# Kernel tuning notes

Hardware: AMD Instinct MI355X
Metric: run time of the kernel (lower is better)

## Reference

```python
import jax, jax.numpy as jnp
import numpy as np

N = 50000   # nodes
E = 800000  # edges (avg degree 16)
H = 128     # hidden_channels
G = 50      # num_gaussians
CUT = 6.0   # cutoff
PI = float(np.pi)
SHIFT = float(np.log(2.0))


def ssp(x):
    # ShiftedSoftplus
    return jax.nn.softplus(x) - SHIFT


def setup_inputs() -> dict:
    key = jax.random.key(0)
    ks = jax.random.split(key, 32)
    p = lambda k, shape: jax.random.normal(k, shape, jnp.float32) * 0.05
    inp = {
        "z": jax.random.normal(ks[0], (N, 3), jnp.float32),
        "dist": jax.random.uniform(ks[1], (E,), jnp.float32) * CUT,
        "edge_index": jax.random.randint(ks[2], (2, E), 0, N, dtype=jnp.int32),
        "init_w": p(ks[3], (3, H)), "init_b": jnp.zeros((H,), jnp.float32),
        # layer 0
        "e0_lin_w": p(ks[4], (H, H)),
        "e0_m0_w": p(ks[5], (G, H)), "e0_m0_b": jnp.zeros((H,), jnp.float32),
        "e0_m2_w": p(ks[6], (H, H)), "e0_m2_b": jnp.zeros((H,), jnp.float32),
        "v0_l1_w": p(ks[7], (H, H)), "v0_l1_b": jnp.zeros((H,), jnp.float32),
        "v0_l2_w": p(ks[8], (H, H)), "v0_l2_b": jnp.zeros((H,), jnp.float32),
        # layer 1
        "e1_lin_w": p(ks[9], (H, H)),
        "e1_m0_w": p(ks[10], (G, H)), "e1_m0_b": jnp.zeros((H,), jnp.float32),
        "e1_m2_w": p(ks[11], (H, H)), "e1_m2_b": jnp.zeros((H,), jnp.float32),
        "v1_l1_w": p(ks[12], (H, H)), "v1_l1_b": jnp.zeros((H,), jnp.float32),
        "v1_l2_w": p(ks[13], (H, H)), "v1_l2_b": jnp.zeros((H,), jnp.float32),
        # readout
        "u_l1_w": p(ks[14], (H, H)), "u_l1_b": jnp.zeros((H,), jnp.float32),
        "u_l2_w": p(ks[15], (H, 3)), "u_l2_b": jnp.zeros((3,), jnp.float32),
    }
    return inp


def reference(z, dist, edge_index, init_w, init_b,
              e0_lin_w, e0_m0_w, e0_m0_b, e0_m2_w, e0_m2_b,
              v0_l1_w, v0_l1_b, v0_l2_w, v0_l2_b,
              e1_lin_w, e1_m0_w, e1_m0_b, e1_m2_w, e1_m2_b,
              v1_l1_w, v1_l1_b, v1_l2_w, v1_l2_b,
              u_l1_w, u_l1_b, u_l2_w, u_l2_b):
    n = z.shape[0]
    j, i = edge_index[0], edge_index[1]  # source, target

    # RBF embedding of dist.to(long)  (torch truncates toward zero)
    offset = jnp.linspace(0.0, CUT, G, dtype=jnp.float32)
    coeff = -0.5 / (offset[1] - offset[0]) ** 2
    demb = jnp.exp(coeff * (jnp.trunc(dist)[:, None] - offset[None, :]) ** 2)  # [E,G]

    # cosine cutoff gate
    C = 0.5 * (jnp.cos(dist * (PI / CUT)) + 1.0)  # [E]

    v = z @ init_w + init_b  # [N,H]

    layers = [
        (e0_lin_w, e0_m0_w, e0_m0_b, e0_m2_w, e0_m2_b, v0_l1_w, v0_l1_b, v0_l2_w, v0_l2_b),
        (e1_lin_w, e1_m0_w, e1_m0_b, e1_m2_w, e1_m2_b, v1_l1_w, v1_l1_b, v1_l2_w, v1_l2_b),
    ]
    for lin_w, m0_w, m0_b, m2_w, m2_b, l1_w, l1_b, l2_w, l2_b in layers:
        # update_e: filter MLP on RBF, gated by cutoff, times gathered node feats
        W = (ssp(demb @ m0_w + m0_b) @ m2_w + m2_b) * C[:, None]  # [E,H]
        e = (v @ lin_w)[j] * W                                     # [E,H]
        # update_v: scatter-add into target nodes, then node MLP + residual
        agg = jax.ops.segment_sum(e, i, num_segments=n)            # [N,H]
        v = v + (ssp(agg @ l1_w + l1_b) @ l2_w + l2_b)

    # update_u readout
    return ssp(v @ u_l1_w + u_l1_b) @ u_l2_w + u_l2_b  # [N,3]
```

## Files before the change

### kernel.cpp

```cpp
#include <hip/hip_runtime.h>
#include <cstdint>
#include <cstddef>

#define HD 128
#define GD 50
static constexpr float PI_F   = 3.14159265358979323846f;
static constexpr float CUTF   = 6.0f;
static constexpr float SHIFTF = 0.69314718055994530942f;

typedef _Float16 f16x8 __attribute__((ext_vector_type(8)));
typedef _Float16 f16x2 __attribute__((ext_vector_type(2)));
typedef float    f32x4 __attribute__((ext_vector_type(4)));

struct Ptr8 { const float* p[8]; };

__device__ __forceinline__ float ssp(float x) {
    float e = __expf(-fabsf(x));
    return fmaxf(x, 0.0f) + __logf(1.0f + e) - SHIFTF;
}

__device__ __forceinline__ _Float16* t16(_Float16* base, int row, int byte) {
    return (_Float16*)((char*)base + row * 256 + (byte ^ ((row & 7) << 4)));
}

__device__ __forceinline__ void mfma32(const f16x8 af[4],
                                       const _Float16* __restrict__ Bf,
                                       int lane, f32x4 acc[8]) {
    #pragma unroll
    for (int ks = 0; ks < 4; ++ks)
        #pragma unroll
        for (int ct = 0; ct < 8; ++ct)
            acc[ct] = __builtin_amdgcn_mfma_f32_16x16x32_f16(
                af[ks], ((const f16x8*)Bf)[(ct * 4 + ks) * 64 + lane], acc[ct], 0, 0, 0);
}

template <int ACT>
__device__ __forceinline__ void acc_to_t16(const f32x4 acc[8], const float* bias,
                                           int lane, _Float16* tile) {
    int col0 = lane & 15, r0 = (lane >> 4) * 4;
    #pragma unroll
    for (int ct = 0; ct < 8; ++ct) {
        int c = ct * 16 + col0;
        float bs = bias ? bias[c] : 0.f;
        #pragma unroll
        for (int r = 0; r < 4; ++r) {
            float o = acc[ct][r] + bs;
            if (ACT) o = ssp(o);
            *t16(tile, r0 + r, c * 2) = (_Float16)o;
        }
    }
}

__device__ __forceinline__ void t16_to_af(_Float16* tile, int lane, f16x8 af[4]) {
    int row = lane & 15, kgB = (lane >> 4) * 16;
    #pragma unroll
    for (int ks = 0; ks < 4; ++ks)
        af[ks] = *(const f16x8*)t16(tile, row, ks * 64 + kgB);
}

__device__ __forceinline__ void t16_store(_Float16* tile, _Float16* g,
                                          int rowbase, int lane, int n) {
    #pragma unroll
    for (int it = 0; it < 4; ++it) {
        int f8 = it * 64 + lane;
        int row = f8 >> 4, g8 = f8 & 15;
        f16x8 h = *(const f16x8*)t16(tile, row, g8 * 16);
        if (rowbase + row < n) ((f16x8*)g)[(size_t)(rowbase + row) * 16 + g8] = h;
    }
}

__device__ __forceinline__ void vz_acc(const float* __restrict__ z,
                                       const float* __restrict__ iw,
                                       const float* __restrict__ ib,
                                       int rowbase, int lane, int n,
                                       f32x4 vz[8]) {
    int col0 = lane & 15, r0 = (lane >> 4) * 4;
    float zr[4][3];
    #pragma unroll
    for (int r = 0; r < 4; ++r) {
        int row = min(rowbase + r0 + r, n - 1);
        zr[r][0] = z[row * 3 + 0];
        zr[r][1] = z[row * 3 + 1];
        zr[r][2] = z[row * 3 + 2];
    }
    #pragma unroll
    for (int ct = 0; ct < 8; ++ct) {
        int c = ct * 16 + col0;
        float w0 = iw[c], w1 = iw[HD + c], w2 = iw[2 * HD + c], bz = ib[c];
        #pragma unroll
        for (int r = 0; r < 4; ++r)
            vz[ct][r] = fmaf(zr[r][0], w0, fmaf(zr[r][1], w1, fmaf(zr[r][2], w2, bz)));
    }
}

__global__ __launch_bounds__(HD) void k_wtab2(Ptr8 P, float* __restrict__ wtab) {
    const int bin = blockIdx.x, layer = blockIdx.y;
    const int t = threadIdx.x;
    const float* m0w = P.p[layer * 4 + 0];
    const float* m0b = P.p[layer * 4 + 1];
    const float* m2w = P.p[layer * 4 + 2];
    const float* m2b = P.p[layer * 4 + 3];
    __shared__ float hbuf[HD];

    const float spacing = CUTF / (GD - 1);
    const float coeff   = -0.5f / (spacing * spacing);

    float acc = m0b[t];
    #pragma unroll 5
    for (int g = 0; g < GD; ++g) {
        float d = (float)bin - (float)g * spacing;
        acc = fmaf(__expf(coeff * d * d), m0w[g * HD + t], acc);
    }
    hbuf[t] = ssp(acc);
    __syncthreads();

    float acc2 = m2b[t];
    #pragma unroll 8
    for (int k = 0; k < HD; ++k)
        acc2 = fmaf(hbuf[k], m2w[k * HD + t], acc2);
    wtab[(layer * 7 + bin) * HD + t] = acc2;
}

__global__ __launch_bounds__(256) void k_prepB7(Ptr8 P, _Float16* __restrict__ Bf) {
    int slot = blockIdx.y;
    const float* W = P.p[slot];
    int idx = blockIdx.x * 256 + threadIdx.x;
    if (idx >= 2048) return;
    int l  = idx & 63;
    int f  = idx >> 6;
    int ks = f & 3, ct = f >> 2;
    int col = ct * 16 + (l & 15);
    int k0  = ks * 32 + ((l >> 4) << 3);
    f16x8 o;
    #pragma unroll
    for (int j = 0; j < 8; ++j) o[j] = (_Float16)W[(size_t)(k0 + j) * HD + col];
    ((f16x8*)(Bf + (size_t)slot * 16384))[idx] = o;
}

__global__ __launch_bounds__(256) void k_deg(const int* __restrict__ ei,
                                             int* __restrict__ deg, int nedges) {
    int e = blockIdx.x * 256 + threadIdx.x;
    if (e < nedges) atomicAdd(&deg[ei[nedges + e]], 1);
}

__global__ __launch_bounds__(1024) void k_scan1(const int* __restrict__ deg,
                                                int* __restrict__ rowstart,
                                                int* __restrict__ blocksum, int n) {
    __shared__ int wsum[16];
    int tid  = threadIdx.x;
    int lane = tid & 63, wid = tid >> 6;
    int i = blockIdx.x * 1024 + tid;
    int val = (i < n) ? deg[i] : 0;
    int x = val;
    #pragma unroll
    for (int off = 1; off < 64; off <<= 1) {
        int y = __shfl_up(x, off, 64);
        if (lane >= off) x += y;
    }
    if (lane == 63) wsum[wid] = x;
    __syncthreads();
    if (wid == 0) {
        int s = (lane < 16) ? wsum[lane] : 0;
        #pragma unroll
        for (int off = 1; off < 16; off <<= 1) {
            int y = __shfl_up(s, off, 64);
            if (lane >= off) s += y;
        }
        if (lane < 16) wsum[lane] = s;
    }
    __syncthreads();
    int wbase = (wid > 0) ? wsum[wid - 1] : 0;
    if (i <= n) rowstart[i] = wbase + x - val;
    if (tid == 1023) blocksum[blockIdx.x] = wsum[15];
}

__global__ __launch_bounds__(64) void k_scan2(int* __restrict__ blocksum, int nb) {
    int lane = threadIdx.x;
    int v = (lane < nb) ? blocksum[lane] : 0;
    int x = v;
    #pragma unroll
    for (int off = 1; off < 64; off <<= 1) {
        int y = __shfl_up(x, off, 64);
        if (lane >= off) x += y;
    }
    if (lane < nb) blocksum[lane] = x - v;
}

__global__ __launch_bounds__(1024) void k_scan3(int* __restrict__ rowstart,
                                                int* __restrict__ cursor,
                                                const int* __restrict__ blocksum,
                                                int n) {
    int i = blockIdx.x * 1024 + threadIdx.x;
    if (i <= n) {
        int rs = rowstart[i] + blocksum[blockIdx.x];
        rowstart[i] = rs;
        if (i < n) cursor[i] = rs;
    }
}

__global__ __launch_bounds__(256) void k_escatter(const int* __restrict__ ei,
                                                  const float* __restrict__ dist,
                                                  int* __restrict__ cursor,
                                                  int2* __restrict__ ecomb,
                                                  int nedges) {
    int e = blockIdx.x * 256 + threadIdx.x;
    if (e >= nedges) return;
    int   j = ei[e];
    int   i = ei[nedges + e];
    float d = dist[e];
    int bin = min((int)d, 6);
    float Cg = 0.5f * (cosf(d * (PI_F / CUTF)) + 1.0f);
    int pos = atomicAdd(&cursor[i], 1);
    ecomb[pos] = make_int2(j | (bin << 25), __float_as_int(Cg));
}

__global__ __launch_bounds__(256) void k_agg(const int* __restrict__ rowstart,
                                             const int2* __restrict__ ecomb,
                                             const _Float16* __restrict__ vlin_h,
                                             const float* __restrict__ wtab,
                                             _Float16* __restrict__ agg_h, int n) {
    __shared__ float lwt[7 * HD];
    int tid = threadIdx.x;
    if (tid < 224) ((float4*)lwt)[tid] = ((const float4*)wtab)[tid];
    __syncthreads();

    int node = blockIdx.x * 4 + (tid >> 6);
    if (node >= n) return;
    int lane = tid & 63;
    int beg = rowstart[node], end = rowstart[node + 1];

    float accx = 0.f, accy = 0.f;
    const float* lwt2 = lwt + 2 * lane;
    int e = beg;
    for (; e + 3 < end; e += 4) {
        int2 c0 = ecomb[e],     c1 = ecomb[e + 1];
        int2 c2 = ecomb[e + 2], c3 = ecomb[e + 3];
        f16x2 h0 = *(const f16x2*)(vlin_h + (size_t)(c0.x & 0x01FFFFFF) * HD + 2 * lane);
        f16x2 h1 = *(const f16x2*)(vlin_h + (size_t)(c1.x & 0x01FFFFFF) * HD + 2 * lane);
        f16x2 h2 = *(const f16x2*)(vlin_h + (size_t)(c2.x & 0x01FFFFFF) * HD + 2 * lane);
        f16x2 h3 = *(const f16x2*)(vlin_h + (size_t)(c3.x & 0x01FFFFFF) * HD + 2 * lane);
        float2 w0 = *(const float2*)(lwt2 + (c0.x >> 25) * HD);
        float2 w1 = *(const float2*)(lwt2 + (c1.x >> 25) * HD);
        float2 w2 = *(const float2*)(lwt2 + (c2.x >> 25) * HD);
        float2 w3 = *(const float2*)(lwt2 + (c3.x >> 25) * HD);
        float g0 = __int_as_float(c0.y), g1 = __int_as_float(c1.y);
        float g2 = __int_as_float(c2.y), g3 = __int_as_float(c3.y);
        accx = fmaf((float)h0[0], w0.x * g0, accx);
        accy = fmaf((float)h0[1], w0.y * g0, accy);
        accx = fmaf((float)h1[0], w1.x * g1, accx);
        accy = fmaf((float)h1[1], w1.y * g1, accy);
        accx = fmaf((float)h2[0], w2.x * g2, accx);
        accy = fmaf((float)h2[1], w2.y * g2, accy);
        accx = fmaf((float)h3[0], w3.x * g3, accx);
        accy = fmaf((float)h3[1], w3.y * g3, accy);
    }
    for (; e < end; ++e) {
        int2 c0 = ecomb[e];
        f16x2 h0 = *(const f16x2*)(vlin_h + (size_t)(c0.x & 0x01FFFFFF) * HD + 2 * lane);
        float2 w0 = *(const float2*)(lwt2 + (c0.x >> 25) * HD);
        float g0 = __int_as_float(c0.y);
        accx = fmaf((float)h0[0], w0.x * g0, accx);
        accy = fmaf((float)h0[1], w0.y * g0, accy);
    }
    f16x2 o; o[0] = (_Float16)accx; o[1] = (_Float16)accy;
    *(f16x2*)(agg_h + (size_t)node * HD + 2 * lane) = o;
}

__global__ __launch_bounds__(256) void k_front(const float* __restrict__ z,
                                               const float* __restrict__ iw,
                                               const float* __restrict__ ib,
                                               const _Float16* __restrict__ BfL,
                                               _Float16* __restrict__ vlin_h, int n) {
    __shared__ __attribute__((aligned(16))) _Float16 ldsh[4][2048];
    int tid = threadIdx.x, lane = tid & 63, wid = tid >> 6;
    int rowbase = blockIdx.x * 64 + wid * 16;
    _Float16* tile16 = ldsh[wid];

    int arow = min(rowbase + (lane & 15), n - 1);
    float z0 = z[arow * 3 + 0], z1 = z[arow * 3 + 1], z2 = z[arow * 3 + 2];
    int kg = (lane >> 4) * 8;

    f16x8 af[4];
    #pragma unroll
    for (int ks = 0; ks < 4; ++ks) {
        f16x8 h;
        #pragma unroll
        for (int j = 0; j < 8; ++j) {
            int c = ks * 32 + kg + j;
            h[j] = (_Float16)fmaf(z0, iw[c], fmaf(z1, iw[HD + c], fmaf(z2, iw[2 * HD + c], ib[c])));
        }
        af[ks] = h;
    }

    f32x4 acc[8];
    #pragma unroll
    for (int i = 0; i < 8; ++i) acc[i] = (f32x4){0.f, 0.f, 0.f, 0.f};
    mfma32(af, BfL, lane, acc);
    acc_to_t16<0>(acc, nullptr, lane, tile16);
    __syncthreads();
    t16_store(tile16, vlin_h, rowbase, lane, n);
}

__global__ __launch_bounds__(256) void k_mid(const _Float16* __restrict__ agg_h,
                                             const _Float16* __restrict__ Bf1,
                                             const float* __restrict__ b1,
                                             const _Float16* __restrict__ Bf2,
                                             const float* __restrict__ b2,
                                             const _Float16* __restrict__ BfL,
                                             const float* __restrict__ z,
                                             const float* __restrict__ iw,
                                             const float* __restrict__ ib,
                                             f32x4* __restrict__ vres4,
                                             _Float16* __restrict__ vlin_h, int n) {
    __shared__ __attribute__((aligned(16))) _Float16 ldsh[4][2048];
    int tid = threadIdx.x, lane = tid & 63, wid = tid >> 6;
    int rowbase = blockIdx.x * 64 + wid * 16;
    _Float16* tile16 = ldsh[wid];

    int arow = min(rowbase + (lane & 15), n - 1);
    int kg = (lane >> 4) * 8;
    f16x8 af[4];
    #pragma unroll
    for (int ks = 0; ks < 4; ++ks)
        af[ks] = *(const f16x8*)(agg_h + (size_t)arow * HD + ks * 32 + kg);

    f32x4 acc[8];
    #pragma unroll
    for (int i = 0; i < 8; ++i) acc[i] = (f32x4){0.f, 0.f, 0.f, 0.f};
    mfma32(af, Bf1, lane, acc);
    acc_to_t16<1>(acc, b1, lane, tile16);
    __syncthreads();
    t16_to_af(tile16, lane, af);

    #pragma unroll
    for (int i = 0; i < 8; ++i) acc[i] = (f32x4){0.f, 0.f, 0.f, 0.f};
    mfma32(af, Bf2, lane, acc);

    f32x4 vz[8];
    vz_acc(z, iw, ib, rowbase, lane, n, vz);
    int col0 = lane & 15;
    #pragma unroll
    for (int ct = 0; ct < 8; ++ct) {
        float bs = b2[ct * 16 + col0];
        #pragma unroll
        for (int r = 0; r < 4; ++r) acc[ct][r] += bs + vz[ct][r];
        size_t g = ((size_t)(blockIdx.x * 4 + wid) * 8 + ct) * 64 + lane;
        vres4[g] = acc[ct];
    }

    acc_to_t16<0>(acc, nullptr, lane, tile16);
    __syncthreads();
    t16_to_af(tile16, lane, af);

    #pragma unroll
    for (int i = 0; i < 8; ++i) acc[i] = (f32x4){0.f, 0.f, 0.f, 0.f};
    mfma32(af, BfL, lane, acc);
    acc_to_t16<0>(acc, nullptr, lane, tile16);
    __syncthreads();
    t16_store(tile16, vlin_h, rowbase, lane, n);
}

__global__ __launch_bounds__(256) void k_back(const _Float16* __restrict__ agg_h,
                                              const _Float16* __restrict__ Bf1,
                                              const float* __restrict__ b1,
                                              const _Float16* __restrict__ Bf2,
                                              const float* __restrict__ b2,
                                              const _Float16* __restrict__ BfU,
                                              const float* __restrict__ ub1,
                                              const float* __restrict__ w2,
                                              const float* __restrict__ ub2,
                                              const f32x4* __restrict__ vres4,
                                              float* __restrict__ out, int n) {
    __shared__ __attribute__((aligned(16))) _Float16 ldsh[4][2048];
    int tid = threadIdx.x, lane = tid & 63, wid = tid >> 6;
    int rowbase = blockIdx.x * 64 + wid * 16;
    _Float16* tile16 = ldsh[wid];

    int arow = min(rowbase + (lane & 15), n - 1);
    int kg = (lane >> 4) * 8;
    f16x8 af[4];
    #pragma unroll
    for (int ks = 0; ks < 4; ++ks)
        af[ks] = *(const f16x8*)(agg_h + (size_t)arow * HD + ks * 32 + kg);

    f32x4 acc[8];
    #pragma unroll
    for (int i = 0; i < 8; ++i) acc[i] = (f32x4){0.f, 0.f, 0.f, 0.f};
    mfma32(af, Bf1, lane, acc);
    acc_to_t16<1>(acc, b1, lane, tile16);
    __syncthreads();
    t16_to_af(tile16, lane, af);

    #pragma unroll
    for (int i = 0; i < 8; ++i) acc[i] = (f32x4){0.f, 0.f, 0.f, 0.f};
    mfma32(af, Bf2, lane, acc);

    int col0 = lane & 15;
    #pragma unroll
    for (int ct = 0; ct < 8; ++ct) {
        float bs = b2[ct * 16 + col0];
        f32x4 rv = vres4[((size_t)(blockIdx.x * 4 + wid) * 8 + ct) * 64 + lane];
        #pragma unroll
        for (int r = 0; r < 4; ++r) acc[ct][r] += bs + rv[r];
    }

    acc_to_t16<0>(acc, nullptr, lane, tile16);
    __syncthreads();
    t16_to_af(tile16, lane, af);

    #pragma unroll
    for (int i = 0; i < 8; ++i) acc[i] = (f32x4){0.f, 0.f, 0.f, 0.f};
    mfma32(af, BfU, lane, acc);

    int r0 = (lane >> 4) * 4;
    float p0[4] = {0.f, 0.f, 0.f, 0.f};
    float p1[4] = {0.f, 0.f, 0.f, 0.f};
    float p2[4] = {0.f, 0.f, 0.f, 0.f};
    #pragma unroll
    for (int ct = 0; ct < 8; ++ct) {
        int c = ct * 16 + col0;
        float bu = ub1[c];
        float w20 = w2[c * 3 + 0], w21 = w2[c * 3 + 1], w22 = w2[c * 3 + 2];
        #pragma unroll
        for (int r = 0; r < 4; ++r) {
            float u = ssp(acc[ct][r] + bu);
            p0[r] = fmaf(u, w20, p0[r]);
            p1[r] = fmaf(u, w21, p1[r]);
            p2[r] = fmaf(u, w22, p2[r]);
        }
    }
    #pragma unroll
    for (int m = 1; m < 16; m <<= 1) {
        #pragma unroll
        for (int r = 0; r < 4; ++r) {
            p0[r] += __shfl_xor(p0[r], m, 64);
            p1[r] += __shfl_xor(p1[r], m, 64);
            p2[r] += __shfl_xor(p2[r], m, 64);
        }
    }
    if (col0 == 0) {
        #pragma unroll
        for (int r = 0; r < 4; ++r) {
            int row = rowbase + r0 + r;
            if (row < n) {
                out[(size_t)row * 3 + 0] = p0[r] + ub2[0];
                out[(size_t)row * 3 + 1] = p1[r] + ub2[1];
                out[(size_t)row * 3 + 2] = p2[r] + ub2[2];
            }
        }
    }
}

extern "C" void kernel_launch(void* const* d_in, const int* in_sizes, int n_in,
                              void* d_out, int out_size, void* d_ws, size_t ws_size,
                              hipStream_t stream) {
    const float* z      = (const float*)d_in[0];
    const float* dist   = (const float*)d_in[1];
    const int*   ei     = (const int*)d_in[2];
    const float* init_w = (const float*)d_in[3];
    const float* init_b = (const float*)d_in[4];

    const float* L[2][9];
    for (int l = 0; l < 2; ++l)
        for (int p = 0; p < 9; ++p)
            L[l][p] = (const float*)d_in[5 + l * 9 + p];

    const float* u_l1_w = (const float*)d_in[23];
    const float* u_l1_b = (const float*)d_in[24];
    const float* u_l2_w = (const float*)d_in[25];
    const float* u_l2_b = (const float*)d_in[26];
    float* out = (float*)d_out;

    const int N = in_sizes[0] / 3;
    const int E = in_sizes[1];

    const int mmGrid   = (N + 63) / 64;
    const int edgeGrid = (E + 255) / 256;
    const int scanB    = (N + 1 + 1023) / 1024;
    const int aggGrid  = (N + 3) / 4;

    float* wtab   = (float*)d_ws;
    float* bf     = wtab + 2048;
    float* vres   = bf + 57344;
    float* vh     = vres + (size_t)mmGrid * 8192;
    float* aggh   = vh + (size_t)N * 64;
    int2*  ecomb  = (int2*)(aggh + (size_t)N * 64);
    int*   deg    = (int*)(ecomb + E);
    int*   rowstart = deg + N;
    int*   cursor = rowstart + N + 1;
    int*   blocksum = cursor + N;

    _Float16* vlin_h = (_Float16*)vh;
    _Float16* agg_h  = (_Float16*)aggh;
    f32x4*    vres4  = (f32x4*)vres;
    _Float16* Bf     = (_Float16*)bf;
    _Float16* BfW[7];
    for (int i = 0; i < 7; ++i) BfW[i] = Bf + (size_t)i * 16384;

    Ptr8 wt; wt.p[0] = L[0][1]; wt.p[1] = L[0][2]; wt.p[2] = L[0][3]; wt.p[3] = L[0][4];
             wt.p[4] = L[1][1]; wt.p[5] = L[1][2]; wt.p[6] = L[1][3]; wt.p[7] = L[1][4];
    k_wtab2<<<dim3(7, 2), HD, 0, stream>>>(wt, wtab);

    Ptr8 pb; pb.p[0] = L[0][0]; pb.p[1] = L[0][5]; pb.p[2] = L[0][7];
             pb.p[3] = L[1][0]; pb.p[4] = L[1][5]; pb.p[5] = L[1][7];
             pb.p[6] = u_l1_w;  pb.p[7] = u_l1_w;
    k_prepB7<<<dim3(8, 7), 256, 0, stream>>>(pb, Bf);

    hipMemsetAsync(deg, 0, (size_t)N * sizeof(int), stream);
    k_deg<<<edgeGrid, 256, 0, stream>>>(ei, deg, E);
    k_scan1<<<scanB, 1024, 0, stream>>>(deg, rowstart, blocksum, N);
    k_scan2<<<1, 64, 0, stream>>>(blocksum, scanB);
    k_scan3<<<scanB, 1024, 0, stream>>>(rowstart, cursor, blocksum, N);
    k_escatter<<<edgeGrid, 256, 0, stream>>>(ei, dist, cursor, ecomb, E);

    k_front<<<mmGrid, 256, 0, stream>>>(z, init_w, init_b, BfW[0], vlin_h, N);
    k_agg<<<aggGrid, 256, 0, stream>>>(rowstart, ecomb, vlin_h, wtab, agg_h, N);
    k_mid<<<mmGrid, 256, 0, stream>>>(agg_h, BfW[1], L[0][6], BfW[2], L[0][8],
                                      BfW[3], z, init_w, init_b, vres4, vlin_h, N);
    k_agg<<<aggGrid, 256, 0, stream>>>(rowstart, ecomb, vlin_h, wtab + 7 * HD, agg_h, N);
    k_back<<<mmGrid, 256, 0, stream>>>(agg_h, BfW[4], L[1][6], BfW[5], L[1][8],
                                       BfW[6], u_l1_b, u_l2_w, u_l2_b, vres4, out, N);
}
```

Measured before the change: 362.5 us.

## Fuse edge scatter with front matmul, split node MLPs across waves by column

Zeroing the degree array moves into an extra slice of the weight-prep kernel, which removes the memset. The edge-scatter kernel and the initial node projection kernel become one launch, with block ranges dispatched to either job, so the two can overlap. The node MLP kernels (front, mid, back) now give each 64-row block's work to 16-row blocks whose four waves each compute two column tiles. This raises block count and cuts per-wave register use, at the cost of extra barriers and an LDS cross-wave reduction for the readout.

```diff
diff --git a/kernel.cpp b/kernel.cpp
--- a/kernel.cpp
+++ b/kernel.cpp
@@ -23,30 +23,31 @@
     return (_Float16*)((char*)base + row * 256 + (byte ^ ((row & 7) << 4)));
 }
 
-__device__ __forceinline__ void mfma32(const f16x8 af[4],
-                                       const _Float16* __restrict__ Bf,
-                                       int lane, f32x4 acc[8]) {
+__device__ __forceinline__ void mfma_ct(const f16x8 af[4],
+                                        const _Float16* __restrict__ Bf,
+                                        int lane, f32x4 acc[2], int ctb) {
     #pragma unroll
     for (int ks = 0; ks < 4; ++ks)
         #pragma unroll
-        for (int ct = 0; ct < 8; ++ct)
-            acc[ct] = __builtin_amdgcn_mfma_f32_16x16x32_f16(
-                af[ks], ((const f16x8*)Bf)[(ct * 4 + ks) * 64 + lane], acc[ct], 0, 0, 0);
+        for (int c = 0; c < 2; ++c)
+            acc[c] = __builtin_amdgcn_mfma_f32_16x16x32_f16(
+                af[ks], ((const f16x8*)Bf)[((ctb + c) * 4 + ks) * 64 + lane],
+                acc[c], 0, 0, 0);
 }
 
 template <int ACT>
-__device__ __forceinline__ void acc_to_t16(const f32x4 acc[8], const float* bias,
-                                           int lane, _Float16* tile) {
+__device__ __forceinline__ void acc_to_t16_ct(const f32x4 acc[2], const float* bias,
+                                              int lane, _Float16* tile, int ctb) {
     int col0 = lane & 15, r0 = (lane >> 4) * 4;
     #pragma unroll
-    for (int ct = 0; ct < 8; ++ct) {
-        int c = ct * 16 + col0;
-        float bs = bias ? bias[c] : 0.f;
+    for (int c = 0; c < 2; ++c) {
+        int cc = (ctb + c) * 16 + col0;
+        float bs = bias ? bias[cc] : 0.f;
         #pragma unroll
         for (int r = 0; r < 4; ++r) {
-            float o = acc[ct][r] + bs;
+            float o = acc[c][r] + bs;
             if (ACT) o = ssp(o);
-            *t16(tile, r0 + r, c * 2) = (_Float16)o;
+            *t16(tile, r0 + r, cc * 2) = (_Float16)o;
         }
     }
 }
@@ -58,22 +59,11 @@
         af[ks] = *(const f16x8*)t16(tile, row, ks * 64 + kgB);
 }
 
-__device__ __forceinline__ void t16_store(_Float16* tile, _Float16* g,
-                                          int rowbase, int lane, int n) {
-    #pragma unroll
-    for (int it = 0; it < 4; ++it) {
-        int f8 = it * 64 + lane;
-        int row = f8 >> 4, g8 = f8 & 15;
-        f16x8 h = *(const f16x8*)t16(tile, row, g8 * 16);
-        if (rowbase + row < n) ((f16x8*)g)[(size_t)(rowbase + row) * 16 + g8] = h;
-    }
-}
-
-__device__ __forceinline__ void vz_acc(const float* __restrict__ z,
-                                       const float* __restrict__ iw,
-                                       const float* __restrict__ ib,
-                                       int rowbase, int lane, int n,
-                                       f32x4 vz[8]) {
+__device__ __forceinline__ void vz_ct(const float* __restrict__ z,
+                                      const float* __restrict__ iw,
+                                      const float* __restrict__ ib,
+                                      int rowbase, int lane, int n, int ctb,
+                                      f32x4 vz[2]) {
     int col0 = lane & 15, r0 = (lane >> 4) * 4;
     float zr[4][3];
     #pragma unroll
@@ -84,12 +74,12 @@
         zr[r][2] = z[row * 3 + 2];
     }
     #pragma unroll
-    for (int ct = 0; ct < 8; ++ct) {
-        int c = ct * 16 + col0;
-        float w0 = iw[c], w1 = iw[HD + c], w2 = iw[2 * HD + c], bz = ib[c];
+    for (int c = 0; c < 2; ++c) {
+        int cc = (ctb + c) * 16 + col0;
+        float w0 = iw[cc], w1 = iw[HD + cc], w2 = iw[2 * HD + cc], bz = ib[cc];
         #pragma unroll
         for (int r = 0; r < 4; ++r)
-            vz[ct][r] = fmaf(zr[r][0], w0, fmaf(zr[r][1], w1, fmaf(zr[r][2], w2, bz)));
+            vz[c][r] = fmaf(zr[r][0], w0, fmaf(zr[r][1], w1, fmaf(zr[r][2], w2, bz)));
     }
 }
 
@@ -121,11 +111,16 @@
     wtab[(layer * 7 + bin) * HD + t] = acc2;
 }
 
-__global__ __launch_bounds__(256) void k_prepB7(Ptr8 P, _Float16* __restrict__ Bf) {
+__global__ __launch_bounds__(256) void k_prepB7(Ptr8 P, _Float16* __restrict__ Bf,
+                                                int* __restrict__ deg, int n) {
     int slot = blockIdx.y;
+    int idx = blockIdx.x * 256 + threadIdx.x;
+    if (slot == 7) {
+        for (int i = idx; i < n; i += 2048) deg[i] = 0;
+        return;
+    }
+    if (idx >= 2048) return;
     const float* W = P.p[slot];
-    int idx = blockIdx.x * 256 + threadIdx.x;
-    if (idx >= 2048) return;
     int l  = idx & 63;
     int f  = idx >> 6;
     int ks = f & 3, ct = f >> 2;
@@ -198,20 +193,64 @@
     }
 }
 
-__global__ __launch_bounds__(256) void k_escatter(const int* __restrict__ ei,
+__global__ __launch_bounds__(256) void k_fused_fe(const int* __restrict__ ei,
                                                   const float* __restrict__ dist,
                                                   int* __restrict__ cursor,
                                                   int2* __restrict__ ecomb,
-                                                  int nedges) {
-    int e = blockIdx.x * 256 + threadIdx.x;
-    if (e >= nedges) return;
-    int   j = ei[e];
-    int   i = ei[nedges + e];
-    float d = dist[e];
-    int bin = min((int)d, 6);
-    float Cg = 0.5f * (cosf(d * (PI_F / CUTF)) + 1.0f);
-    int pos = atomicAdd(&cursor[i], 1);
-    ecomb[pos] = make_int2(j | (bin << 25), __float_as_int(Cg));
+                                                  int nedges, int escGrid,
+                                                  const float* __restrict__ z,
+                                                  const float* __restrict__ iw,
+                                                  const float* __restrict__ ib,
+                                                  const _Float16* __restrict__ BfL,
+                                                  _Float16* __restrict__ vlin_h,
+                                                  int n) {
+    __shared__ __attribute__((aligned(16))) _Float16 tile16[2048];
+    int bx = blockIdx.x;
+    if (bx < escGrid) {
+        int base = bx * 1024 + (int)threadIdx.x;
+        #pragma unroll
+        for (int k = 0; k < 4; ++k) {
+            int e = base + k * 256;
+            if (e < nedges) {
+                int   j = ei[e];
+                int   i = ei[nedges + e];
+                float d = dist[e];
+                int bin = min((int)d, 6);
+                float Cg = 0.5f * (cosf(d * (PI_F / CUTF)) + 1.0f);
+                int pos = atomicAdd(&cursor[i], 1);
+                ecomb[pos] = make_int2(j | (bin << 25), __float_as_int(Cg));
+            }
+        }
+        return;
+    }
+    int tid = threadIdx.x, lane = tid & 63, wid = tid >> 6;
+    int rowbase = (bx - escGrid) * 16;
+    int arow = min(rowbase + (lane & 15), n - 1);
+    float z0 = z[arow * 3 + 0], z1 = z[arow * 3 + 1], z2 = z[arow * 3 + 2];
+    int kg = (lane >> 4) * 8;
+
+    f16x8 af[4];
+    #pragma unroll
+    for (int ks = 0; ks < 4; ++ks) {
+        f16x8 h;
+        #pragma unroll
+        for (int j = 0; j < 8; ++j) {
+            int c = ks * 32 + kg + j;
+            h[j] = (_Float16)fmaf(z0, iw[c], fmaf(z1, iw[HD + c], fmaf(z2, iw[2 * HD + c], ib[c])));
+        }
+        af[ks] = h;
+    }
+
+    f32x4 acc[2];
+    acc[0] = (f32x4){0.f, 0.f, 0.f, 0.f};
+    acc[1] = (f32x4){0.f, 0.f, 0.f, 0.f};
+    mfma_ct(af, BfL, lane, acc, wid * 2);
+    acc_to_t16_ct<0>(acc, nullptr, lane, tile16, wid * 2);
+    __syncthreads();
+    int row = tid >> 4, g8 = tid & 15;
+    if (rowbase + row < n)
+        ((f16x8*)vlin_h)[(size_t)(rowbase + row) * 16 + g8] =
+            *(const f16x8*)t16(tile16, row, g8 * 16);
 }
 
 __global__ __launch_bounds__(256) void k_agg(const int* __restrict__ rowstart,
@@ -266,41 +305,6 @@
     *(f16x2*)(agg_h + (size_t)node * HD + 2 * lane) = o;
 }
 
-__global__ __launch_bounds__(256) void k_front(const float* __restrict__ z,
-                                               const float* __restrict__ iw,
-                                               const float* __restrict__ ib,
-                                               const _Float16* __restrict__ BfL,
-                                               _Float16* __restrict__ vlin_h, int n) {
-    __shared__ __attribute__((aligned(16))) _Float16 ldsh[4][2048];
-    int tid = threadIdx.x, lane = tid & 63, wid = tid >> 6;
-    int rowbase = blockIdx.x * 64 + wid * 16;
-    _Float16* tile16 = ldsh[wid];
-
-    int arow = min(rowbase + (lane & 15), n - 1);
-    float z0 = z[arow * 3 + 0], z1 = z[arow * 3 + 1], z2 = z[arow * 3 + 2];
-    int kg = (lane >> 4) * 8;
-
-    f16x8 af[4];
-    #pragma unroll
-    for (int ks = 0; ks < 4; ++ks) {
-        f16x8 h;
-        #pragma unroll
-        for (int j = 0; j < 8; ++j) {
-            int c = ks * 32 + kg + j;
-            h[j] = (_Float16)fmaf(z0, iw[c], fmaf(z1, iw[HD + c], fmaf(z2, iw[2 * HD + c], ib[c])));
-        }
-        af[ks] = h;
-    }
-
-    f32x4 acc[8];
-    #pragma unroll
-    for (int i = 0; i < 8; ++i) acc[i] = (f32x4){0.f, 0.f, 0.f, 0.f};
-    mfma32(af, BfL, lane, acc);
-    acc_to_t16<0>(acc, nullptr, lane, tile16);
-    __syncthreads();
-    t16_store(tile16, vlin_h, rowbase, lane, n);
-}
-
 __global__ __launch_bounds__(256) void k_mid(const _Float16* __restrict__ agg_h,
                                              const _Float16* __restrict__ Bf1,
                                              const float* __restrict__ b1,
@@ -312,10 +316,10 @@
                                              const float* __restrict__ ib,
                                              f32x4* __restrict__ vres4,
                                              _Float16* __restrict__ vlin_h, int n) {
-    __shared__ __attribute__((aligned(16))) _Float16 ldsh[4][2048];
+    __shared__ __attribute__((aligned(16))) _Float16 tile16[2048];
     int tid = threadIdx.x, lane = tid & 63, wid = tid >> 6;
-    int rowbase = blockIdx.x * 64 + wid * 16;
-    _Float16* tile16 = ldsh[wid];
+    int rowbase = blockIdx.x * 16;
+    int ctb = wid * 2;
 
     int arow = min(rowbase + (lane & 15), n - 1);
     int kg = (lane >> 4) * 8;
@@ -324,40 +328,44 @@
     for (int ks = 0; ks < 4; ++ks)
         af[ks] = *(const f16x8*)(agg_h + (size_t)arow * HD + ks * 32 + kg);
 
-    f32x4 acc[8];
-    #pragma unroll
-    for (int i = 0; i < 8; ++i) acc[i] = (f32x4){0.f, 0.f, 0.f, 0.f};
-    mfma32(af, Bf1, lane, acc);
-    acc_to_t16<1>(acc, b1, lane, tile16);
+    f32x4 acc[2];
+    acc[0] = (f32x4){0.f, 0.f, 0.f, 0.f};
+    acc[1] = (f32x4){0.f, 0.f, 0.f, 0.f};
+    mfma_ct(af, Bf1, lane, acc, ctb);
+    acc_to_t16_ct<1>(acc, b1, lane, tile16, ctb);
     __syncthreads();
     t16_to_af(tile16, lane, af);
-
-    #pragma unroll
-    for (int i = 0; i < 8; ++i) acc[i] = (f32x4){0.f, 0.f, 0.f, 0.f};
-    mfma32(af, Bf2, lane, acc);
-
-    f32x4 vz[8];
-    vz_acc(z, iw, ib, rowbase, lane, n, vz);
+    __syncthreads();
+
+    acc[0] = (f32x4){0.f, 0.f, 0.f, 0.f};
+    acc[1] = (f32x4){0.f, 0.f, 0.f, 0.f};
+    mfma_ct(af, Bf2, lane, acc, ctb);
+
+    f32x4 vz[2];
+    vz_ct(z, iw, ib, rowbase, lane, n, ctb, vz);
     int col0 = lane & 15;
     #pragma unroll
-    for (int ct = 0; ct < 8; ++ct) {
-        float bs = b2[ct * 16 + col0];
-        #pragma unroll
-        for (int r = 0; r < 4; ++r) acc[ct][r] += bs + vz[ct][r];
-        size_t g = ((size_t)(blockIdx.x * 4 + wid) * 8 + ct) * 64 + lane;
-        vres4[g] = acc[ct];
-    }
-
-    acc_to_t16<0>(acc, nullptr, lane, tile16);
+    for (int c = 0; c < 2; ++c) {
+        float bs = b2[(ctb + c) * 16 + col0];
+        #pragma unroll
+        for (int r = 0; r < 4; ++r) acc[c][r] += bs + vz[c][r];
+        vres4[((size_t)blockIdx.x * 8 + ctb + c) * 64 + lane] = acc[c];
+    }
+
+    acc_to_t16_ct<0>(acc, nullptr, lane, tile16, ctb);
     __syncthreads();
     t16_to_af(tile16, lane, af);
-
-    #pragma unroll
-    for (int i = 0; i < 8; ++i) acc[i] = (f32x4){0.f, 0.f, 0.f, 0.f};
-    mfma32(af, BfL, lane, acc);
-    acc_to_t16<0>(acc, nullptr, lane, tile16);
-    __syncthreads();
-    t16_store(tile16, vlin_h, rowbase, lane, n);
+    __syncthreads();
+
+    acc[0] = (f32x4){0.f, 0.f, 0.f, 0.f};
+    acc[1] = (f32x4){0.f, 0.f, 0.f, 0.f};
+    mfma_ct(af, BfL, lane, acc, ctb);
+    acc_to_t16_ct<0>(acc, nullptr, lane, tile16, ctb);
+    __syncthreads();
+    int row = tid >> 4, g8 = tid & 15;
+    if (rowbase + row < n)
+        ((f16x8*)vlin_h)[(size_t)(rowbase + row) * 16 + g8] =
+            *(const f16x8*)t16(tile16, row, g8 * 16);
 }
 
 __global__ __launch_bounds__(256) void k_back(const _Float16* __restrict__ agg_h,
@@ -371,10 +379,11 @@
                                               const float* __restrict__ ub2,
                                               const f32x4* __restrict__ vres4,
                                               float* __restrict__ out, int n) {
-    __shared__ __attribute__((aligned(16))) _Float16 ldsh[4][2048];
+    __shared__ __attribute__((aligned(16))) _Float16 tile16[2048];
+    __shared__ float red[4][16][3];
     int tid = threadIdx.x, lane = tid & 63, wid = tid >> 6;
-    int rowbase = blockIdx.x * 64 + wid * 16;
-    _Float16* tile16 = ldsh[wid];
+    int rowbase = blockIdx.x * 16;
+    int ctb = wid * 2;
 
     int arow = min(rowbase + (lane & 15), n - 1);
     int kg = (lane >> 4) * 8;
@@ -383,47 +392,48 @@
     for (int ks = 0; ks < 4; ++ks)
         af[ks] = *(const f16x8*)(agg_h + (size_t)arow * HD + ks * 32 + kg);
 
-    f32x4 acc[8];
-    #pragma unroll
-    for (int i = 0; i < 8; ++i) acc[i] = (f32x4){0.f, 0.f, 0.f, 0.f};
-    mfma32(af, Bf1, lane, acc);
-    acc_to_t16<1>(acc, b1, lane, tile16);
+    f32x4 acc[2];
+    acc[0] = (f32x4){0.f, 0.f, 0.f, 0.f};
+    acc[1] = (f32x4){0.f, 0.f, 0.f, 0.f};
+    mfma_ct(af, Bf1, lane, acc, ctb);
+    acc_to_t16_ct<1>(acc, b1, lane, tile16, ctb);
     __syncthreads();
     t16_to_af(tile16, lane, af);
-
-    #pragma unroll
-    for (int i = 0; i < 8; ++i) acc[i] = (f32x4){0.f, 0.f, 0.f, 0.f};
-    mfma32(af, Bf2, lane, acc);
+    __syncthreads();
+
+    acc[0] = (f32x4){0.f, 0.f, 0.f, 0.f};
+    acc[1] = (f32x4){0.f, 0.f, 0.f, 0.f};
+    mfma_ct(af, Bf2, lane, acc, ctb);
 
     int col0 = lane & 15;
     #pragma unroll
-    for (int ct = 0; ct < 8; ++ct) {
-        float bs = b2[ct * 16 + col0];
-        f32x4 rv = vres4[((size_t)(blockIdx.x * 4 + wid) * 8 + ct) * 64 + lane];
-        #pragma unroll
-        for (int r = 0; r < 4; ++r) acc[ct][r] += bs + rv[r];
-    }
-
-    acc_to_t16<0>(acc, nullptr, lane, tile16);
+    for (int c = 0; c < 2; ++c) {
+        float bs = b2[(ctb + c) * 16 + col0];
+        f32x4 rv = vres4[((size_t)blockIdx.x * 8 + ctb + c) * 64 + lane];
+        #pragma unroll
+        for (int r = 0; r < 4; ++r) acc[c][r] += bs + rv[r];
+    }
+
+    acc_to_t16_ct<0>(acc, nullptr, lane, tile16, ctb);
     __syncthreads();
     t16_to_af(tile16, lane, af);
 
-    #pragma unroll
-    for (int i = 0; i < 8; ++i) acc[i] = (f32x4){0.f, 0.f, 0.f, 0.f};
-    mfma32(af, BfU, lane, acc);
+    acc[0] = (f32x4){0.f, 0.f, 0.f, 0.f};
+    acc[1] = (f32x4){0.f, 0.f, 0.f, 0.f};
+    mfma_ct(af, BfU, lane, acc, ctb);
 
     int r0 = (lane >> 4) * 4;
     float p0[4] = {0.f, 0.f, 0.f, 0.f};
     float p1[4] = {0.f, 0.f, 0.f, 0.f};
     float p2[4] = {0.f, 0.f, 0.f, 0.f};
     #pragma unroll
-    for (int ct = 0; ct < 8; ++ct) {
-        int c = ct * 16 + col0;
-        float bu = ub1[c];
-        float w20 = w2[c * 3 + 0], w21 = w2[c * 3 + 1], w22 = w2[c * 3 + 2];
+    for (int c = 0; c < 2; ++c) {
+        int cc = (ctb + c) * 16 + col0;
+        float bu = ub1[cc];
+        float w20 = w2[cc * 3 + 0], w21 = w2[cc * 3 + 1], w22 = w2[cc * 3 + 2];
         #pragma unroll
         for (int r = 0; r < 4; ++r) {
-            float u = ssp(acc[ct][r] + bu);
+            float u = ssp(acc[c][r] + bu);
             p0[r] = fmaf(u, w20, p0[r]);
             p1[r] = fmaf(u, w21, p1[r]);
             p2[r] = fmaf(u, w22, p2[r]);
@@ -441,13 +451,17 @@
     if (col0 == 0) {
         #pragma unroll
         for (int r = 0; r < 4; ++r) {
-            int row = rowbase + r0 + r;
-            if (row < n) {
-                out[(size_t)row * 3 + 0] = p0[r] + ub2[0];
-                out[(size_t)row * 3 + 1] = p1[r] + ub2[1];
-                out[(size_t)row * 3 + 2] = p2[r] + ub2[2];
-            }
-        }
+            red[wid][r0 + r][0] = p0[r];
+            red[wid][r0 + r][1] = p1[r];
+            red[wid][r0 + r][2] = p2[r];
+        }
+    }
+    __syncthreads();
+    if (tid < 48) {
+        int row = tid / 3, c = tid % 3;
+        float s = red[0][row][c] + red[1][row][c] + red[2][row][c] + red[3][row][c];
+        if (rowbase + row < n)
+            out[(size_t)(rowbase + row) * 3 + c] = s + ub2[c];
     }
 }
 
@@ -474,7 +488,8 @@
     const int N = in_sizes[0] / 3;
     const int E = in_sizes[1];
 
-    const int mmGrid   = (N + 63) / 64;
+    const int nb16     = (N + 15) / 16;
+    const int escGrid  = (E + 1023) / 1024;
     const int edgeGrid = (E + 255) / 256;
     const int scanB    = (N + 1 + 1023) / 1024;
     const int aggGrid  = (N + 3) / 4;
@@ -482,7 +497,7 @@
     float* wtab   = (float*)d_ws;
     float* bf     = wtab + 2048;
     float* vres   = bf + 57344;
-    float* vh     = vres + (size_t)mmGrid * 8192;
+    float* vh     = vres + (size_t)nb16 * 2048;
     float* aggh   = vh + (size_t)N * 64;
     int2*  ecomb  = (int2*)(aggh + (size_t)N * 64);
     int*   deg    = (int*)(ecomb + E);
@@ -504,20 +519,20 @@
     Ptr8 pb; pb.p[0] = L[0][0]; pb.p[1] = L[0][5]; pb.p[2] = L[0][7];
              pb.p[3] = L[1][0]; pb.p[4] = L[1][5]; pb.p[5] = L[1][7];
              pb.p[6] = u_l1_w;  pb.p[7] = u_l1_w;
-    k_prepB7<<<dim3(8, 7), 256, 0, stream>>>(pb, Bf);
-
-    hipMemsetAsync(deg, 0, (size_t)N * sizeof(int), stream);
+    k_prepB7<<<dim3(8, 8), 256, 0, stream>>>(pb, Bf, deg, N);
+
     k_deg<<<edgeGrid, 256, 0, stream>>>(ei, deg, E);
     k_scan1<<<scanB, 1024, 0, stream>>>(deg, rowstart, blocksum, N);
     k_scan2<<<1, 64, 0, stream>>>(blocksum, scanB);
     k_scan3<<<scanB, 1024, 0, stream>>>(rowstart, cursor, blocksum, N);
-    k_escatter<<<edgeGrid, 256, 0, stream>>>(ei, dist, cursor, ecomb, E);
-
-    k_front<<<mmGrid, 256, 0, stream>>>(z, init_w, init_b, BfW[0], vlin_h, N);
+
+    k_fused_fe<<<escGrid + nb16, 256, 0, stream>>>(ei, dist, cursor, ecomb, E, escGrid,
+                                                   z, init_w, init_b, BfW[0], vlin_h, N);
+
     k_agg<<<aggGrid, 256, 0, stream>>>(rowstart, ecomb, vlin_h, wtab, agg_h, N);
-    k_mid<<<mmGrid, 256, 0, stream>>>(agg_h, BfW[1], L[0][6], BfW[2], L[0][8],
-                                      BfW[3], z, init_w, init_b, vres4, vlin_h, N);
+    k_mid<<<nb16, 256, 0, stream>>>(agg_h, BfW[1], L[0][6], BfW[2], L[0][8],
+                                    BfW[3], z, init_w, init_b, vres4, vlin_h, N);
     k_agg<<<aggGrid, 256, 0, stream>>>(rowstart, ecomb, vlin_h, wtab + 7 * HD, agg_h, N);
-    k_back<<<mmGrid, 256, 0, stream>>>(agg_h, BfW[4], L[1][6], BfW[5], L[1][8],
-                                       BfW[6], u_l1_b, u_l2_w, u_l2_b, vres4, out, N);
-}
+    k_back<<<nb16, 256, 0, stream>>>(agg_h, BfW[4], L[1][6], BfW[5], L[1][8],
+                                     BfW[6], u_l1_b, u_l2_w, u_l2_b, vres4, out, N);
+}
```

After: 356.4 us. Within noise of the previous version (-1.7%).
